# Kernel optimization log

Measured on AMD Instinct MI355X. Metric: run time of the kernel, lower is better.

## Reference

```python
import jax, jax.numpy as jnp
import numpy as np

N = 50000      # nodes
E = 800000     # edges (before self loops)
F_IN = 64
H = 128
OUT = 1
G = 512        # graphs in batch
NEG_SLOPE = 0.2


def setup_inputs() -> dict:
    key = jax.random.key(0)
    ks = jax.random.split(key, 16)
    s_in = 1.0 / np.sqrt(F_IN)
    s_h = 1.0 / np.sqrt(H)
    return {
        "x": jax.random.normal(ks[0], (N, F_IN), jnp.float32),
        "edge_index": jax.random.randint(ks[1], (2, E), 0, N, jnp.int64),
        "edge_weight": jax.random.uniform(ks[2], (E,), jnp.float32),
        "batch": jnp.sort(jax.random.randint(ks[3], (N,), 0, G, jnp.int64)),
        # GATv2 layer 1 (lin_l, lin_r, att, bias)
        "Wl1": jax.random.normal(ks[4], (F_IN, H), jnp.float32) * s_in,
        "bl1": jnp.zeros((H,), jnp.float32),
        "Wr1": jax.random.normal(ks[5], (F_IN, H), jnp.float32) * s_in,
        "br1": jnp.zeros((H,), jnp.float32),
        "att1": jax.random.normal(ks[6], (H,), jnp.float32) * s_h,
        "b1": jnp.zeros((H,), jnp.float32),
        # GATv2 layer 2
        "Wl2": jax.random.normal(ks[7], (H, H), jnp.float32) * s_h,
        "bl2": jnp.zeros((H,), jnp.float32),
        "Wr2": jax.random.normal(ks[8], (H, H), jnp.float32) * s_h,
        "br2": jnp.zeros((H,), jnp.float32),
        "att2": jax.random.normal(ks[9], (H,), jnp.float32) * s_h,
        "b2": jnp.zeros((H,), jnp.float32),
        # final linear head
        "Wlin": jax.random.normal(ks[10], (H, OUT), jnp.float32) * s_h,
        "blin": jnp.zeros((OUT,), jnp.float32),
    }


def gatv2_conv(x, src, dst, Wl, bl, Wr, br, att, bias):
    """PyG GATv2Conv, heads=1: alpha = softmax_dst(att . leaky_relu(xl[src]+xr[dst]));
    out[dst] = sum alpha * xl[src] + bias. Self loops already in (src, dst)."""
    xl = x @ Wl + bl                       # [N,H]  source transform
    xr = x @ Wr + br                       # [N,H]  destination transform
    e = xl[src] + xr[dst]                  # [Etot,H]
    logits = jax.nn.leaky_relu(e, NEG_SLOPE) @ att   # [Etot]
    # segment softmax over destination nodes (self loops -> every node nonempty)
    m = jax.ops.segment_max(logits, dst, num_segments=N)
    ea = jnp.exp(logits - m[dst])
    denom = jax.ops.segment_sum(ea, dst, num_segments=N)
    alpha = ea / denom[dst]
    out = jax.ops.segment_sum(alpha[:, None] * xl[src], dst, num_segments=N)
    return out + bias


def reference(x, edge_index, edge_weight, batch,
              Wl1, bl1, Wr1, br1, att1, b1,
              Wl2, bl2, Wr2, br2, att2, b2,
              Wlin, blin):
    # add self loops (GATv2Conv default add_self_loops=True); edge_weight unused by GATv2
    loops = jnp.arange(N, dtype=edge_index.dtype)
    src = jnp.concatenate([edge_index[0], loops])
    dst = jnp.concatenate([edge_index[1], loops])

    h = jax.nn.relu(gatv2_conv(x, src, dst, Wl1, bl1, Wr1, br1, att1, b1))
    h = jax.nn.relu(gatv2_conv(h, src, dst, Wl2, bl2, Wr2, br2, att2, b2))

    # global mean pool over graphs
    sums = jax.ops.segment_sum(h, batch, num_segments=G)          # [G,H]
    cnt = jax.ops.segment_sum(jnp.ones((N,), h.dtype), batch, num_segments=G)
    pooled = sums / jnp.maximum(cnt, 1.0)[:, None]

    return pooled @ Wlin + blin                                   # [G,OUT]
```

## Files before the change

### kernel.cpp

```cpp
#include <hip/hip_runtime.h>
#include <hip/hip_fp16.h>
#include <math.h>

#define N_NODES 50000
#define N_EDGES 800000
#define F_IN    64
#define H_DIM   128
#define N_GRAPH 512
#define NEG_SLOPE 0.2f

typedef __attribute__((ext_vector_type(8))) short short8;
typedef __attribute__((ext_vector_type(4))) float f32x4;
typedef __attribute__((ext_vector_type(2))) float f32x2;
typedef _Float16 h2 __attribute__((ext_vector_type(2)));

#define NBIN   196
#define NBLK1  391
#define NBB    (NBIN * NBLK1)
#define SCANA_NB ((NBB + 255) / 256)

__device__ __forceinline__ void bsplit(float v, unsigned short& h, unsigned short& l) {
    unsigned u = __float_as_uint(v);
    h = (unsigned short)(u >> 16);
    float hf = __uint_as_float(u & 0xFFFF0000u);
    float r = v - hf;
    l = (unsigned short)(__float_as_uint(r) >> 16);
}
__device__ __forceinline__ float bjoin(unsigned short h, unsigned short l) {
    return __uint_as_float(((unsigned)h) << 16) + __uint_as_float(((unsigned)l) << 16);
}

#define NB_PW 192
__global__ __launch_bounds__(256) void k_prep(
    const float* __restrict__ Wl1, const float* __restrict__ Wr1,
    const float* __restrict__ Wl2, const float* __restrict__ Wr2,
    const int* __restrict__ dst,
    unsigned short* __restrict__ WThi, unsigned short* __restrict__ WTlo,
    int* __restrict__ lrank, int* __restrict__ bcnt)
{
    __shared__ int cnt_lds[NBIN];
    const int bid = blockIdx.x, tid = threadIdx.x;
    if (bid < NB_PW) {
        int idx = bid * 256 + tid;
        if (idx < 49152) {
            const float* W; int K, li, base, o;
            if (idx < 8192)       { W = Wl1; K = 64;  li = idx;         base = 0;     o = 0; }
            else if (idx < 16384) { W = Wr1; K = 64;  li = idx - 8192;  base = 0;     o = 1; }
            else if (idx < 32768) { W = Wl2; K = 128; li = idx - 16384; base = 16384; o = 0; }
            else                  { W = Wr2; K = 128; li = idx - 32768; base = 16384; o = 1; }
            int c = li / K, k = li - c * K;
            int g = c >> 4, n16 = c & 15;
            int kkblk = k >> 5, quad = (k >> 3) & 3, j = k & 7;
            int off = base + kkblk * 8192 + o * 4096 + g * 512 + (quad * 16 + n16) * 8 + j;
            unsigned short h, l;
            bsplit(W[k * 128 + c], h, l);
            WThi[off] = h; WTlo[off] = l;
        }
    } else {
        const int b2 = bid - NB_PW;
        if (tid < NBIN) cnt_lds[tid] = 0;
        __syncthreads();
#pragma unroll
        for (int it = 0; it < 8; ++it) {
            int e = b2 * 2048 + it * 256 + tid;
            if (e < N_EDGES) {
                int d = dst[e];
                lrank[e] = atomicAdd(&cnt_lds[d >> 8], 1);
            }
        }
        __syncthreads();
        if (tid < NBIN) bcnt[tid * NBLK1 + b2] = cnt_lds[tid];
    }
}

__global__ __launch_bounds__(256) void k_scanA(const int* __restrict__ bcnt,
                                               int* __restrict__ bbase,
                                               int* __restrict__ partials) {
    __shared__ int s[256];
    int t = threadIdx.x, gid = blockIdx.x * 256 + t;
    int v = (gid < NBB) ? bcnt[gid] : 0;
    s[t] = v;
    __syncthreads();
    for (int off = 1; off < 256; off <<= 1) {
        int x = (t >= off) ? s[t - off] : 0;
        __syncthreads();
        s[t] += x;
        __syncthreads();
    }
    if (gid < NBB) bbase[gid] = s[t] - v;
    if (t == 255) partials[blockIdx.x] = s[t];
}

__global__ __launch_bounds__(256) void k_scanB(int* __restrict__ bbase,
                                               const int* __restrict__ partials) {
    __shared__ int red[256];
    const int t = threadIdx.x, b = blockIdx.x;
    int acc = 0;
    for (int j = t; j < b; j += 256) acc += partials[j];
    red[t] = acc;
    __syncthreads();
    for (int off = 128; off > 0; off >>= 1) {
        if (t < off) red[t] += red[t + off];
        __syncthreads();
    }
    int base = red[0];
    int gid = b * 256 + t;
    if (gid < NBB) bbase[gid] += base;
}

__global__ __launch_bounds__(256) void k_bin2(const int* __restrict__ src,
                                              const int* __restrict__ dst,
                                              const int* __restrict__ lrank,
                                              const int* __restrict__ bbase,
                                              unsigned* __restrict__ ebin) {
    int e = blockIdx.x * 256 + threadIdx.x;
    if (e < N_EDGES) {
        int d = dst[e];
        int pos = bbase[(d >> 8) * NBLK1 + (e >> 11)] + lrank[e];
        ebin[pos] = (unsigned)src[e] | ((unsigned)(d & 255) << 16);
    }
}

__global__ __launch_bounds__(256) void k_bin3(const unsigned* __restrict__ ebin,
                                              const int* __restrict__ bbase,
                                              int* __restrict__ offsets,
                                              int* __restrict__ col_src) {
    __shared__ int cnt2[256];
    __shared__ int sc[256];
    __shared__ int cur[256];
    const int b = blockIdx.x, t = threadIdx.x;
    const int lo = bbase[b * NBLK1];
    const int hi = (b == NBIN - 1) ? N_EDGES : bbase[(b + 1) * NBLK1];

    cnt2[t] = 0;
    __syncthreads();
    for (int pos = lo + t; pos < hi; pos += 256) {
        unsigned u = ebin[pos];
        atomicAdd(&cnt2[u >> 16], 1);
    }
    __syncthreads();
    int v = cnt2[t];
    sc[t] = v;
    __syncthreads();
    for (int off = 1; off < 256; off <<= 1) {
        int x = (t >= off) ? sc[t - off] : 0;
        __syncthreads();
        sc[t] += x;
        __syncthreads();
    }
    int myoff = lo + sc[t] - v;
    int node = b * 256 + t;
    if (node < N_NODES) offsets[node] = myoff;
    cur[t] = myoff;
    if (b == NBIN - 1 && t == 0) offsets[N_NODES] = N_EDGES;
    __syncthreads();
    for (int pos = lo + t; pos < hi; pos += 256) {
        unsigned u = ebin[pos];
        int p = atomicAdd(&cur[u >> 16], 1);
        col_src[p] = (int)(u & 0xFFFFu);
    }
}

#define APITCH 40
#define GB_GEMM ((N_NODES + 63) / 64)

template <bool F32SRC>
__device__ __forceinline__ void gemm_body(
    unsigned short* __restrict__ Ah, unsigned short* __restrict__ Al,
    const float* __restrict__ Xf,
    const unsigned short* __restrict__ Xhi, const unsigned short* __restrict__ Xlo,
    const unsigned short* __restrict__ WThi, const unsigned short* __restrict__ WTlo,
    const float* __restrict__ bl, const float* __restrict__ br,
    unsigned short* __restrict__ OL, unsigned short* __restrict__ OR_,
    int K, int blk)
{
    const int tid  = threadIdx.x;
    const int wv   = tid >> 6;
    const int lane = tid & 63;
    const int n16  = lane & 15;
    const int quad = lane >> 4;
    const int row0 = blk * 64;

    f32x4 acc[4][2][2];
#pragma unroll
    for (int r = 0; r < 4; ++r)
#pragma unroll
        for (int c = 0; c < 2; ++c)
#pragma unroll
            for (int o = 0; o < 2; ++o) acc[r][c][o] = (f32x4)0.f;

    for (int kk = 0; kk < K; kk += 32) {
        if (F32SRC) {
            int r = tid >> 2, sub = tid & 3;
            int grow = row0 + r;
            float4 v0 = make_float4(0.f, 0.f, 0.f, 0.f);
            float4 v1 = make_float4(0.f, 0.f, 0.f, 0.f);
            if (grow < N_NODES) {
                const float* s = Xf + (size_t)grow * K + kk + sub * 8;
                v0 = *(const float4*)s;
                v1 = *(const float4*)(s + 4);
            }
            union { unsigned short s[8]; uint4 u; } Hh, Ll;
            bsplit(v0.x, Hh.s[0], Ll.s[0]); bsplit(v0.y, Hh.s[1], Ll.s[1]);
            bsplit(v0.z, Hh.s[2], Ll.s[2]); bsplit(v0.w, Hh.s[3], Ll.s[3]);
            bsplit(v1.x, Hh.s[4], Ll.s[4]); bsplit(v1.y, Hh.s[5], Ll.s[5]);
            bsplit(v1.z, Hh.s[6], Ll.s[6]); bsplit(v1.w, Hh.s[7], Ll.s[7]);
            *(uint4*)(Ah + r * APITCH + sub * 8) = Hh.u;
            *(uint4*)(Al + r * APITCH + sub * 8) = Ll.u;
        } else {
#pragma unroll
            for (int jj = 0; jj < 2; ++jj) {
                int j = tid + jj * 256;
                int part = j >> 8;
                int r = (j & 255) >> 2, sub = j & 3;
                int grow = row0 + r;
                const unsigned short* s = (part ? Xlo : Xhi) + (size_t)grow * K + kk + sub * 8;
                unsigned short* dl = (part ? Al : Ah) + r * APITCH + sub * 8;
                uint4 v = make_uint4(0u, 0u, 0u, 0u);
                if (grow < N_NODES) v = *(const uint4*)s;
                *(uint4*)dl = v;
            }
        }
        __syncthreads();

        const unsigned short* wb_h = WThi + (size_t)(kk >> 5) * 8192;
        const unsigned short* wb_l = WTlo + (size_t)(kk >> 5) * 8192;
        short8 bh[2][2], bo[2][2];
#pragma unroll
        for (int c = 0; c < 2; ++c)
#pragma unroll
            for (int o = 0; o < 2; ++o) {
                size_t off = (size_t)o * 4096 + (size_t)(wv * 2 + c) * 512 + (size_t)lane * 8;
                bh[c][o] = *(const short8*)(wb_h + off);
                bo[c][o] = *(const short8*)(wb_l + off);
            }
#pragma unroll
        for (int r = 0; r < 4; ++r) {
            int rl = r * 16 + n16;
            short8 ah = *(const short8*)(Ah + rl * APITCH + quad * 8);
            short8 al = *(const short8*)(Al + rl * APITCH + quad * 8);
#pragma unroll
            for (int c = 0; c < 2; ++c)
#pragma unroll
                for (int o = 0; o < 2; ++o) {
                    f32x4 t = acc[r][c][o];
                    t = __builtin_amdgcn_mfma_f32_16x16x32_bf16(ah, bh[c][o], t, 0, 0, 0);
                    t = __builtin_amdgcn_mfma_f32_16x16x32_bf16(ah, bo[c][o], t, 0, 0, 0);
                    t = __builtin_amdgcn_mfma_f32_16x16x32_bf16(al, bh[c][o], t, 0, 0, 0);
                    acc[r][c][o] = t;
                }
        }
        __syncthreads();
    }

#pragma unroll
    for (int r = 0; r < 4; ++r)
#pragma unroll
        for (int c = 0; c < 2; ++c)
#pragma unroll
            for (int o = 0; o < 2; ++o) {
                int col = wv * 32 + c * 16 + n16;
                float bb = (o ? br : bl)[col];
                unsigned short* O = o ? OR_ : OL;
#pragma unroll
                for (int g = 0; g < 4; ++g) {
                    int grow = row0 + r * 16 + quad * 4 + g;
                    if (grow < N_NODES) {
                        __half hv = __float2half(acc[r][c][o][g] + bb);
                        O[(size_t)grow * 128 + col] = *(unsigned short*)&hv;
                    }
                }
            }
}

__global__ __launch_bounds__(256, 4) void k_gemm_f32(
    const float* __restrict__ Xf,
    const unsigned short* __restrict__ WThi, const unsigned short* __restrict__ WTlo,
    const float* __restrict__ bl, const float* __restrict__ br,
    unsigned short* __restrict__ OL, unsigned short* __restrict__ OR_, int K)
{
    __shared__ __align__(16) unsigned short Ah[64 * APITCH];
    __shared__ __align__(16) unsigned short Al[64 * APITCH];
    gemm_body<true>(Ah, Al, Xf, nullptr, nullptr, WThi, WTlo, bl, br, OL, OR_, K, blockIdx.x);
}

__global__ __launch_bounds__(256, 4) void k_gemm_mfma(
    const unsigned short* __restrict__ Xhi, const unsigned short* __restrict__ Xlo,
    const unsigned short* __restrict__ WThi, const unsigned short* __restrict__ WTlo,
    const float* __restrict__ bl, const float* __restrict__ br,
    unsigned short* __restrict__ OL, unsigned short* __restrict__ OR_, int K)
{
    __shared__ __align__(16) unsigned short Ah[64 * APITCH];
    __shared__ __align__(16) unsigned short Al[64 * APITCH];
    gemm_body<false>(Ah, Al, nullptr, Xhi, Xlo, WThi, WTlo, bl, br, OL, OR_, K, blockIdx.x);
}

__device__ __forceinline__ float red16dpp(float v) {
    v += __int_as_float(__builtin_amdgcn_update_dpp(
             0, __float_as_int(v), 0xB1, 0xF, 0xF, true));
    v += __int_as_float(__builtin_amdgcn_update_dpp(
             0, __float_as_int(v), 0x4E, 0xF, 0xF, true));
    v += __int_as_float(__builtin_amdgcn_update_dpp(
             0, __float_as_int(v), 0x141, 0xF, 0xF, true));
    v += __int_as_float(__builtin_amdgcn_update_dpp(
             0, __float_as_int(v), 0x140, 0xF, 0xF, true));
    return v;
}

__device__ __forceinline__ float dot8lk_h(uint4 u, const h2 r[4], const h2 a[4]) {
    const h2 ns = { (_Float16)NEG_SLOPE, (_Float16)NEG_SLOPE };
    float s = 0.f;
    h2 x0 = __builtin_bit_cast(h2, u.x);
    h2 x1 = __builtin_bit_cast(h2, u.y);
    h2 x2 = __builtin_bit_cast(h2, u.z);
    h2 x3 = __builtin_bit_cast(h2, u.w);
    h2 e0 = x0 + r[0];
    h2 e1 = x1 + r[1];
    h2 e2 = x2 + r[2];
    h2 e3 = x3 + r[3];
    h2 l0 = __builtin_elementwise_max(e0, e0 * ns);
    h2 l1 = __builtin_elementwise_max(e1, e1 * ns);
    h2 l2 = __builtin_elementwise_max(e2, e2 * ns);
    h2 l3 = __builtin_elementwise_max(e3, e3 * ns);
    s = __builtin_amdgcn_fdot2(l0, a[0], s, false);
    s = __builtin_amdgcn_fdot2(l1, a[1], s, false);
    s = __builtin_amdgcn_fdot2(l2, a[2], s, false);
    s = __builtin_amdgcn_fdot2(l3, a[3], s, false);
    return s;
}

__global__ __launch_bounds__(256) void k_edge(
    const unsigned short* __restrict__ xl, const unsigned short* __restrict__ xr,
    const float* __restrict__ att, const float* __restrict__ bias,
    const int* __restrict__ offsets, const int* __restrict__ col_src,
    unsigned short* __restrict__ outHi, unsigned short* __restrict__ outLo)
{
    int d = blockIdx.x * 4 + (threadIdx.x >> 6);
    if (d >= N_NODES) return;
    const int lane = threadIdx.x & 63;
    const int q = lane >> 4;
    const int t = lane & 15;
    const size_t dim0 = (size_t)t * 8;

    h2 rr[4], aa[4];
    {
        uint4 ur = *(const uint4*)(xr + (size_t)d * 128 + dim0);
        rr[0] = __builtin_bit_cast(h2, ur.x);
        rr[1] = __builtin_bit_cast(h2, ur.y);
        rr[2] = __builtin_bit_cast(h2, ur.z);
        rr[3] = __builtin_bit_cast(h2, ur.w);
        const float4 a0 = *(const float4*)(att + dim0);
        const float4 a1 = *(const float4*)(att + dim0 + 4);
        h2 w0 = { (_Float16)a0.x, (_Float16)a0.y }; aa[0] = w0;
        h2 w1 = { (_Float16)a0.z, (_Float16)a0.w }; aa[1] = w1;
        h2 w2 = { (_Float16)a1.x, (_Float16)a1.y }; aa[2] = w2;
        h2 w3 = { (_Float16)a1.z, (_Float16)a1.w }; aa[3] = w3;
    }

    uint4 uxs = *(const uint4*)(xl + (size_t)d * 128 + dim0);
    float sl = red16dpp(dot8lk_h(uxs, rr, aa));

    float m = sl, thr = sl + 8.f;
    float lsum = (q == 0) ? 1.f : 0.f;
    f32x2 acc[4];
    {
        float2 sa = __half22float2(*(__half2*)&uxs.x);
        float2 sb = __half22float2(*(__half2*)&uxs.y);
        float2 sc_ = __half22float2(*(__half2*)&uxs.z);
        float2 sd = __half22float2(*(__half2*)&uxs.w);
        f32x2 z = {0.f, 0.f};
        f32x2 v0 = {sa.x, sa.y}; acc[0] = (q == 0) ? v0 : z;
        f32x2 v1 = {sb.x, sb.y}; acc[1] = (q == 0) ? v1 : z;
        f32x2 v2 = {sc_.x, sc_.y}; acc[2] = (q == 0) ? v2 : z;
        f32x2 v3 = {sd.x, sd.y}; acc[3] = (q == 0) ? v3 : z;
    }

    const int ibeg = offsets[d], iend = offsets[d + 1];
    int ia = ibeg + q;
    bool vA = ia < iend;
    int sA = vA ? col_src[ia] : d;
    uint4 uA = *(const uint4*)(xl + (size_t)sA * 128 + dim0);
    int ib = ia + 4;
    bool vB = ib < iend;
    int sB = vB ? col_src[ib] : d;

    for (int base = ibeg; base < iend; base += 4) {
        uint4 uB = *(const uint4*)(xl + (size_t)sB * 128 + dim0);
        int ic = base + 8 + q;
        bool vC = ic < iend;
        int sC = vC ? col_src[ic] : d;

        float logit = red16dpp(dot8lk_h(uA, rr, aa));
        if (__builtin_expect(logit > thr, 0)) {
            float sc = __expf(m - logit);
            lsum *= sc;
#pragma unroll
            for (int j = 0; j < 4; ++j) acc[j] = acc[j] * sc;
            m = logit; thr = logit + 8.f;
        }
        float w = vA ? __expf(logit - m) : 0.f;
        lsum += w;
        {
            __half2* hp = (__half2*)&uA;
#pragma unroll
            for (int j = 0; j < 4; ++j) {
                float2 xf = __half22float2(hp[j]);
                acc[j].x = fmaf(xf.x, w, acc[j].x);
                acc[j].y = fmaf(xf.y, w, acc[j].y);
            }
        }

        uA = uB; vA = vB; sB = sC; vB = vC;
    }

    float M = m;
    M = fmaxf(M, __shfl_xor(M, 16));
    M = fmaxf(M, __shfl_xor(M, 32));
    float sc = __expf(m - M);
    lsum *= sc;
    f32x2 sc2 = {sc, sc};
#pragma unroll
    for (int j = 0; j < 4; ++j) acc[j] = acc[j] * sc2;
#pragma unroll
    for (int off = 16; off <= 32; off <<= 1) {
        lsum += __shfl_xor(lsum, off);
#pragma unroll
        for (int j = 0; j < 4; ++j) {
            acc[j].x += __shfl_xor(acc[j].x, off);
            acc[j].y += __shfl_xor(acc[j].y, off);
        }
    }

    if (q == 0) {
        float inv = 1.f / lsum;
        const float4 b0 = *(const float4*)(bias + dim0);
        const float4 b1 = *(const float4*)(bias + dim0 + 4);
        float bv[8] = {b0.x, b0.y, b0.z, b0.w, b1.x, b1.y, b1.z, b1.w};
        float v[8];
#pragma unroll
        for (int j = 0; j < 4; ++j) {
            v[2 * j]     = fmaxf(fmaf(acc[j].x, inv, bv[2 * j]), 0.f);
            v[2 * j + 1] = fmaxf(fmaf(acc[j].y, inv, bv[2 * j + 1]), 0.f);
        }
        union { unsigned short s[8]; uint4 u; } Hh, Ll;
#pragma unroll
        for (int i2 = 0; i2 < 8; ++i2) bsplit(v[i2], Hh.s[i2], Ll.s[i2]);
        *(uint4*)(outHi + (size_t)d * 128 + dim0) = Hh.u;
        *(uint4*)(outLo + (size_t)d * 128 + dim0) = Ll.u;
    }
}

__global__ __launch_bounds__(256) void k_pool(
    const unsigned short* __restrict__ hHi, const unsigned short* __restrict__ hLo,
    const int* __restrict__ batch,
    float* __restrict__ psum, float* __restrict__ pcnt)
{
    const int tid = threadIdx.x;
    const int tx = tid & 31;
    const int ty = tid >> 5;
    const int n0 = blockIdx.x * 64;
    const int d0 = tx * 4;

    float4 acc = make_float4(0.f, 0.f, 0.f, 0.f);
    int cur = -1, crun = 0;
#pragma unroll
    for (int it = 0; it < 8; ++it) {
        int n = n0 + it * 8 + ty;
        if (n < N_NODES) {
            int g = batch[n];
            if (g != cur) {
                if (cur >= 0) {
                    atomicAdd(&psum[cur * 128 + d0 + 0], acc.x);
                    atomicAdd(&psum[cur * 128 + d0 + 1], acc.y);
                    atomicAdd(&psum[cur * 128 + d0 + 2], acc.z);
                    atomicAdd(&psum[cur * 128 + d0 + 3], acc.w);
                    if (tx == 0) atomicAdd(&pcnt[cur], (float)crun);
                }
                cur = g; acc = make_float4(0.f, 0.f, 0.f, 0.f); crun = 0;
            }
            ushort4 h = *(const ushort4*)(hHi + (size_t)n * 128 + d0);
            ushort4 l = *(const ushort4*)(hLo + (size_t)n * 128 + d0);
            acc.x += bjoin(h.x, l.x);
            acc.y += bjoin(h.y, l.y);
            acc.z += bjoin(h.z, l.z);
            acc.w += bjoin(h.w, l.w);
            crun++;
        }
    }
    if (cur >= 0) {
        atomicAdd(&psum[cur * 128 + d0 + 0], acc.x);
        atomicAdd(&psum[cur * 128 + d0 + 1], acc.y);
        atomicAdd(&psum[cur * 128 + d0 + 2], acc.z);
        atomicAdd(&psum[cur * 128 + d0 + 3], acc.w);
        if (tx == 0) atomicAdd(&pcnt[cur], (float)crun);
    }
}

__global__ __launch_bounds__(256) void k_head(
    const float* __restrict__ psum, const float* __restrict__ pcnt,
    const float* __restrict__ Wlin, const float* __restrict__ blin,
    float* __restrict__ out)
{
    int g = blockIdx.x * 4 + (threadIdx.x >> 6);
    if (g >= N_GRAPH) return;
    int lane = threadIdx.x & 63;
    float c = fmaxf(pcnt[g], 1.f);
    float2 s = *(const float2*)(psum + (size_t)g * 128 + lane * 2);
    float p = (s.x * Wlin[lane * 2] + s.y * Wlin[lane * 2 + 1]) / c;
#pragma unroll
    for (int off = 32; off > 0; off >>= 1) p += __shfl_xor(p, off);
    if (lane == 0) out[g] = p + blin[0];
}

extern "C" void kernel_launch(void* const* d_in, const int* in_sizes, int n_in,
                              void* d_out, int out_size, void* d_ws, size_t ws_size,
                              hipStream_t stream) {
    const float* x     = (const float*)d_in[0];
    const int*   ei    = (const int*)d_in[1];
    const int*   batch = (const int*)d_in[3];
    const float* Wl1 = (const float*)d_in[4],  *bl1 = (const float*)d_in[5];
    const float* Wr1 = (const float*)d_in[6],  *br1 = (const float*)d_in[7];
    const float* att1= (const float*)d_in[8],  *b1  = (const float*)d_in[9];
    const float* Wl2 = (const float*)d_in[10], *bl2 = (const float*)d_in[11];
    const float* Wr2 = (const float*)d_in[12], *br2 = (const float*)d_in[13];
    const float* att2= (const float*)d_in[14], *b2  = (const float*)d_in[15];
    const float* Wlin= (const float*)d_in[16], *blin= (const float*)d_in[17];
    float* out = (float*)d_out;

    const int* src = ei;
    const int* dst = ei + N_EDGES;

    char* p = (char*)d_ws;
    auto carve = [&](size_t bytes) {
        void* r = (void*)p;
        p += (bytes + 255) & ~(size_t)255;
        return r;
    };
    unsigned short* bufA   = (unsigned short*)carve((size_t)N_NODES * 128 * 2);
    unsigned short* bufB   = (unsigned short*)carve((size_t)N_NODES * 128 * 2);
    unsigned short* Hhi    = (unsigned short*)carve((size_t)N_NODES * 128 * 2);
    unsigned short* Hlo    = (unsigned short*)carve((size_t)N_NODES * 128 * 2);
    unsigned short* WThi   = (unsigned short*)carve(49152 * 2);
    unsigned short* WTlo   = (unsigned short*)carve(49152 * 2);
    int*            offsets= (int*)carve((size_t)(N_NODES + 1) * 4);
    int*            lrank  = (int*)carve((size_t)N_EDGES * 4);
    int*            bcnt   = (int*)carve((size_t)NBB * 4);
    int*            bbase  = (int*)carve((size_t)NBB * 4);
    int*            partials=(int*)carve(SCANA_NB * 4);
    unsigned*       ebin   = (unsigned*)carve((size_t)N_EDGES * 4);
    int*            col_src= (int*)carve((size_t)N_EDGES * 4);
    char* zb = (char*)carve(262144 + 2048);
    float* psum   = (float*)zb;
    float* pcnt   = (float*)(zb + 262144);
    const size_t zbytes = 262144 + 2048;

    hipMemsetAsync(zb, 0, zbytes, stream);

    k_prep<<<NB_PW + NBLK1, 256, 0, stream>>>(
        Wl1, Wr1, Wl2, Wr2, dst, WThi, WTlo, lrank, bcnt);

    k_gemm_f32<<<GB_GEMM, 256, 0, stream>>>(x, WThi, WTlo,
                                            bl1, br1, bufA, bufB, F_IN);

    k_scanA<<<SCANA_NB, 256, 0, stream>>>(bcnt, bbase, partials);
    k_scanB<<<SCANA_NB, 256, 0, stream>>>(bbase, partials);
    k_bin2 <<<(N_EDGES + 255) / 256, 256, 0, stream>>>(src, dst, lrank, bbase, ebin);
    k_bin3 <<<NBIN, 256, 0, stream>>>(ebin, bbase, offsets, col_src);

    k_edge<<<(N_NODES + 3) / 4, 256, 0, stream>>>(
        bufA, bufB, att1, b1, offsets, col_src, Hhi, Hlo);
    k_gemm_mfma<<<GB_GEMM, 256, 0, stream>>>(Hhi, Hlo, WThi + 16384, WTlo + 16384,
                                             bl2, br2, bufA, bufB, H_DIM);
    k_edge<<<(N_NODES + 3) / 4, 256, 0, stream>>>(
        bufA, bufB, att2, b2, offsets, col_src, Hhi, Hlo);
    k_pool<<<(N_NODES + 63) / 64, 256, 0, stream>>>(Hhi, Hlo, batch, psum, pcnt);
    k_head<<<(N_GRAPH + 3) / 4, 256, 0, stream>>>(psum, pcnt, Wlin, blin, out);
}
```

Before: 273.7 us.

## Store hidden activations in fp16 and use single fp16 MFMA for layer-2 GEMM

The hidden activations between layers were stored as a split bf16 hi/lo pair, and the layer-2 GEMM ran extra MFMAs to recover near-fp32 precision. They are now stored as a single fp16 tensor, and layer 2 uses one fp16 MFMA per tile with fp16 weights. This halves the activation writes in the edge kernel and the reads in the GEMM and pool kernels, and cuts the layer-2 MFMA count. The cost is lower precision in the hidden features and layer-2 weights, which could affect accuracy tolerance.

```diff
diff --git a/kernel.cpp b/kernel.cpp
--- a/kernel.cpp
+++ b/kernel.cpp
@@ -13,6 +13,7 @@
 typedef __attribute__((ext_vector_type(4))) float f32x4;
 typedef __attribute__((ext_vector_type(2))) float f32x2;
 typedef _Float16 h2 __attribute__((ext_vector_type(2)));
+typedef _Float16 h8 __attribute__((ext_vector_type(8)));
 
 #define NBIN   196
 #define NBLK1  391
@@ -26,9 +27,6 @@
     float r = v - hf;
     l = (unsigned short)(__float_as_uint(r) >> 16);
 }
-__device__ __forceinline__ float bjoin(unsigned short h, unsigned short l) {
-    return __uint_as_float(((unsigned)h) << 16) + __uint_as_float(((unsigned)l) << 16);
-}
 
 #define NB_PW 192
 __global__ __launch_bounds__(256) void k_prep(
@@ -36,6 +34,7 @@
     const float* __restrict__ Wl2, const float* __restrict__ Wr2,
     const int* __restrict__ dst,
     unsigned short* __restrict__ WThi, unsigned short* __restrict__ WTlo,
+    unsigned short* __restrict__ WT2f,
     int* __restrict__ lrank, int* __restrict__ bcnt)
 {
     __shared__ int cnt_lds[NBIN];
@@ -52,9 +51,15 @@
             int g = c >> 4, n16 = c & 15;
             int kkblk = k >> 5, quad = (k >> 3) & 3, j = k & 7;
             int off = base + kkblk * 8192 + o * 4096 + g * 512 + (quad * 16 + n16) * 8 + j;
-            unsigned short h, l;
-            bsplit(W[k * 128 + c], h, l);
-            WThi[off] = h; WTlo[off] = l;
+            float wv = W[k * 128 + c];
+            if (base == 0) {
+                unsigned short h, l;
+                bsplit(wv, h, l);
+                WThi[off] = h; WTlo[off] = l;
+            } else {
+                __half hv = __float2half(wv);
+                WT2f[off - 16384] = *(unsigned short*)&hv;
+            }
         }
     } else {
         const int b2 = bid - NB_PW;
@@ -164,22 +169,21 @@
 #define APITCH 40
 #define GB_GEMM ((N_NODES + 63) / 64)
 
-template <bool F32SRC>
-__device__ __forceinline__ void gemm_body(
-    unsigned short* __restrict__ Ah, unsigned short* __restrict__ Al,
+__global__ __launch_bounds__(256, 4) void k_gemm_f32(
     const float* __restrict__ Xf,
-    const unsigned short* __restrict__ Xhi, const unsigned short* __restrict__ Xlo,
     const unsigned short* __restrict__ WThi, const unsigned short* __restrict__ WTlo,
     const float* __restrict__ bl, const float* __restrict__ br,
-    unsigned short* __restrict__ OL, unsigned short* __restrict__ OR_,
-    int K, int blk)
+    unsigned short* __restrict__ OL, unsigned short* __restrict__ OR_, int K)
 {
+    __shared__ __align__(16) unsigned short Ah[64 * APITCH];
+    __shared__ __align__(16) unsigned short Al[64 * APITCH];
+
     const int tid  = threadIdx.x;
     const int wv   = tid >> 6;
     const int lane = tid & 63;
     const int n16  = lane & 15;
     const int quad = lane >> 4;
-    const int row0 = blk * 64;
+    const int row0 = blockIdx.x * 64;
 
     f32x4 acc[4][2][2];
 #pragma unroll
@@ -190,7 +194,7 @@
             for (int o = 0; o < 2; ++o) acc[r][c][o] = (f32x4)0.f;
 
     for (int kk = 0; kk < K; kk += 32) {
-        if (F32SRC) {
+        {
             int r = tid >> 2, sub = tid & 3;
             int grow = row0 + r;
             float4 v0 = make_float4(0.f, 0.f, 0.f, 0.f);
@@ -207,19 +211,6 @@
             bsplit(v1.z, Hh.s[6], Ll.s[6]); bsplit(v1.w, Hh.s[7], Ll.s[7]);
             *(uint4*)(Ah + r * APITCH + sub * 8) = Hh.u;
             *(uint4*)(Al + r * APITCH + sub * 8) = Ll.u;
-        } else {
-#pragma unroll
-            for (int jj = 0; jj < 2; ++jj) {
-                int j = tid + jj * 256;
-                int part = j >> 8;
-                int r = (j & 255) >> 2, sub = j & 3;
-                int grow = row0 + r;
-                const unsigned short* s = (part ? Xlo : Xhi) + (size_t)grow * K + kk + sub * 8;
-                unsigned short* dl = (part ? Al : Ah) + r * APITCH + sub * 8;
-                uint4 v = make_uint4(0u, 0u, 0u, 0u);
-                if (grow < N_NODES) v = *(const uint4*)s;
-                *(uint4*)dl = v;
-            }
         }
         __syncthreads();
 
@@ -273,26 +264,81 @@
             }
 }
 
-__global__ __launch_bounds__(256, 4) void k_gemm_f32(
-    const float* __restrict__ Xf,
-    const unsigned short* __restrict__ WThi, const unsigned short* __restrict__ WTlo,
+__global__ __launch_bounds__(256, 4) void k_gemm_f16(
+    const unsigned short* __restrict__ X,
+    const unsigned short* __restrict__ WT2f,
     const float* __restrict__ bl, const float* __restrict__ br,
-    unsigned short* __restrict__ OL, unsigned short* __restrict__ OR_, int K)
+    unsigned short* __restrict__ OL, unsigned short* __restrict__ OR_)
 {
     __shared__ __align__(16) unsigned short Ah[64 * APITCH];
-    __shared__ __align__(16) unsigned short Al[64 * APITCH];
-    gemm_body<true>(Ah, Al, Xf, nullptr, nullptr, WThi, WTlo, bl, br, OL, OR_, K, blockIdx.x);
-}
-
-__global__ __launch_bounds__(256, 4) void k_gemm_mfma(
-    const unsigned short* __restrict__ Xhi, const unsigned short* __restrict__ Xlo,
-    const unsigned short* __restrict__ WThi, const unsigned short* __restrict__ WTlo,
-    const float* __restrict__ bl, const float* __restrict__ br,
-    unsigned short* __restrict__ OL, unsigned short* __restrict__ OR_, int K)
-{
-    __shared__ __align__(16) unsigned short Ah[64 * APITCH];
-    __shared__ __align__(16) unsigned short Al[64 * APITCH];
-    gemm_body<false>(Ah, Al, nullptr, Xhi, Xlo, WThi, WTlo, bl, br, OL, OR_, K, blockIdx.x);
+
+    const int tid  = threadIdx.x;
+    const int wv   = tid >> 6;
+    const int lane = tid & 63;
+    const int n16  = lane & 15;
+    const int quad = lane >> 4;
+    const int row0 = blockIdx.x * 64;
+
+    f32x4 acc[4][2][2];
+#pragma unroll
+    for (int r = 0; r < 4; ++r)
+#pragma unroll
+        for (int c = 0; c < 2; ++c)
+#pragma unroll
+            for (int o = 0; o < 2; ++o) acc[r][c][o] = (f32x4)0.f;
+
+    for (int kk = 0; kk < 128; kk += 32) {
+        {
+            int r = tid >> 2, sub = tid & 3;
+            int grow = row0 + r;
+            uint4 v = make_uint4(0u, 0u, 0u, 0u);
+            if (grow < N_NODES)
+                v = *(const uint4*)(X + (size_t)grow * 128 + kk + sub * 8);
+            *(uint4*)(Ah + r * APITCH + sub * 8) = v;
+        }
+        __syncthreads();
+
+        const unsigned short* wb = WT2f + (size_t)(kk >> 5) * 8192;
+        h8 bf[2][2];
+#pragma unroll
+        for (int c = 0; c < 2; ++c)
+#pragma unroll
+            for (int o = 0; o < 2; ++o) {
+                size_t off = (size_t)o * 4096 + (size_t)(wv * 2 + c) * 512 + (size_t)lane * 8;
+                bf[c][o] = *(const h8*)(wb + off);
+            }
+#pragma unroll
+        for (int r = 0; r < 4; ++r) {
+            int rl = r * 16 + n16;
+            h8 ah = *(const h8*)(Ah + rl * APITCH + quad * 8);
+#pragma unroll
+            for (int c = 0; c < 2; ++c)
+#pragma unroll
+                for (int o = 0; o < 2; ++o)
+                    acc[r][c][o] = __builtin_amdgcn_mfma_f32_16x16x32_f16(
+                        ah, bf[c][o], acc[r][c][o], 0, 0, 0);
+        }
+        __syncthreads();
+    }
+
+#pragma unroll
+    for (int r = 0; r < 4; ++r)
+#pragma unroll
+        for (int c = 0; c < 2; ++c)
+#pragma unroll
+            for (int o = 0; o < 2; ++o) {
+                int col = wv * 32 + c * 16 + n16;
+                float bb = (o ? br : bl)[col];
+                unsigned short* O = o ? OR_ : OL;
+#pragma unroll
+                for (int g = 0; g < 4; ++g) {
+                    int grow = row0 + r * 16 + quad * 4 + g;
+                    if (grow < N_NODES) {
+                        __half hv = __float2half(acc[r][c][o][g] + bb);
+                        O[(size_t)grow * 128 + col] = *(unsigned short*)&hv;
+                    }
+                }
+            }
 }
 
 __device__ __forceinline__ float red16dpp(float v) {
@@ -333,7 +379,7 @@
     const unsigned short* __restrict__ xl, const unsigned short* __restrict__ xr,
     const float* __restrict__ att, const float* __restrict__ bias,
     const int* __restrict__ offsets, const int* __restrict__ col_src,
-    unsigned short* __restrict__ outHi, unsigned short* __restrict__ outLo)
+    unsigned short* __restrict__ outH)
 {
     int d = blockIdx.x * 4 + (threadIdx.x >> 6);
     if (d >= N_NODES) return;
@@ -436,22 +482,19 @@
         const float4 b0 = *(const float4*)(bias + dim0);
         const float4 b1 = *(const float4*)(bias + dim0 + 4);
         float bv[8] = {b0.x, b0.y, b0.z, b0.w, b1.x, b1.y, b1.z, b1.w};
-        float v[8];
+        union { __half2 h[4]; uint4 u; } O;
 #pragma unroll
         for (int j = 0; j < 4; ++j) {
-            v[2 * j]     = fmaxf(fmaf(acc[j].x, inv, bv[2 * j]), 0.f);
-            v[2 * j + 1] = fmaxf(fmaf(acc[j].y, inv, bv[2 * j + 1]), 0.f);
-        }
-        union { unsigned short s[8]; uint4 u; } Hh, Ll;
-#pragma unroll
-        for (int i2 = 0; i2 < 8; ++i2) bsplit(v[i2], Hh.s[i2], Ll.s[i2]);
-        *(uint4*)(outHi + (size_t)d * 128 + dim0) = Hh.u;
-        *(uint4*)(outLo + (size_t)d * 128 + dim0) = Ll.u;
+            float v0 = fmaxf(fmaf(acc[j].x, inv, bv[2 * j]), 0.f);
+            float v1 = fmaxf(fmaf(acc[j].y, inv, bv[2 * j + 1]), 0.f);
+            O.h[j] = __floats2half2_rn(v0, v1);
+        }
+        *(uint4*)(outH + (size_t)d * 128 + dim0) = O.u;
     }
 }
 
 __global__ __launch_bounds__(256) void k_pool(
-    const unsigned short* __restrict__ hHi, const unsigned short* __restrict__ hLo,
+    const unsigned short* __restrict__ H,
     const int* __restrict__ batch,
     float* __restrict__ psum, float* __restrict__ pcnt)
 {
@@ -478,12 +521,10 @@
                 }
                 cur = g; acc = make_float4(0.f, 0.f, 0.f, 0.f); crun = 0;
             }
-            ushort4 h = *(const ushort4*)(hHi + (size_t)n * 128 + d0);
-            ushort4 l = *(const ushort4*)(hLo + (size_t)n * 128 + d0);
-            acc.x += bjoin(h.x, l.x);
-            acc.y += bjoin(h.y, l.y);
-            acc.z += bjoin(h.z, l.z);
-            acc.w += bjoin(h.w, l.w);
+            uint2 hv = *(const uint2*)(H + (size_t)n * 128 + d0);
+            float2 a = __half22float2(*(__half2*)&hv.x);
+            float2 b = __half22float2(*(__half2*)&hv.y);
+            acc.x += a.x; acc.y += a.y; acc.z += b.x; acc.w += b.y;
             crun++;
         }
     }
@@ -538,10 +579,10 @@
     };
     unsigned short* bufA   = (unsigned short*)carve((size_t)N_NODES * 128 * 2);
     unsigned short* bufB   = (unsigned short*)carve((size_t)N_NODES * 128 * 2);
-    unsigned short* Hhi    = (unsigned short*)carve((size_t)N_NODES * 128 * 2);
-    unsigned short* Hlo    = (unsigned short*)carve((size_t)N_NODES * 128 * 2);
-    unsigned short* WThi   = (unsigned short*)carve(49152 * 2);
-    unsigned short* WTlo   = (unsigned short*)carve(49152 * 2);
+    unsigned short* H      = (unsigned short*)carve((size_t)N_NODES * 128 * 2);
+    unsigned short* WThi   = (unsigned short*)carve(16384 * 2);
+    unsigned short* WTlo   = (unsigned short*)carve(16384 * 2);
+    unsigned short* WT2f   = (unsigned short*)carve(32768 * 2);
     int*            offsets= (int*)carve((size_t)(N_NODES + 1) * 4);
     int*            lrank  = (int*)carve((size_t)N_EDGES * 4);
     int*            bcnt   = (int*)carve((size_t)NBB * 4);
@@ -557,7 +598,7 @@
     hipMemsetAsync(zb, 0, zbytes, stream);
 
     k_prep<<<NB_PW + NBLK1, 256, 0, stream>>>(
-        Wl1, Wr1, Wl2, Wr2, dst, WThi, WTlo, lrank, bcnt);
+        Wl1, Wr1, Wl2, Wr2, dst, WThi, WTlo, WT2f, lrank, bcnt);
 
     k_gemm_f32<<<GB_GEMM, 256, 0, stream>>>(x, WThi, WTlo,
                                             bl1, br1, bufA, bufB, F_IN);
@@ -568,11 +609,10 @@
     k_bin3 <<<NBIN, 256, 0, stream>>>(ebin, bbase, offsets, col_src);
 
     k_edge<<<(N_NODES + 3) / 4, 256, 0, stream>>>(
-        bufA, bufB, att1, b1, offsets, col_src, Hhi, Hlo);
-    k_gemm_mfma<<<GB_GEMM, 256, 0, stream>>>(Hhi, Hlo, WThi + 16384, WTlo + 16384,
-                                             bl2, br2, bufA, bufB, H_DIM);
+        bufA, bufB, att1, b1, offsets, col_src, H);
+    k_gemm_f16<<<GB_GEMM, 256, 0, stream>>>(H, WT2f, bl2, br2, bufA, bufB);
     k_edge<<<(N_NODES + 3) / 4, 256, 0, stream>>>(
-        bufA, bufB, att2, b2, offsets, col_src, Hhi, Hlo);
-    k_pool<<<(N_NODES + 63) / 64, 256, 0, stream>>>(Hhi, Hlo, batch, psum, pcnt);
+        bufA, bufB, att2, b2, offsets, col_src, H);
+    k_pool<<<(N_NODES + 63) / 64, 256, 0, stream>>>(H, batch, psum, pcnt);
     k_head<<<(N_GRAPH + 3) / 4, 256, 0, stream>>>(psum, pcnt, Wlin, blin, out);
 }
```

Result: faster. 258.2 us (-5.7%).
